# Optimization experiments

Hardware: AMD Instinct MI355X
Metric: run time of the kernel (lower is better)

The kernel has to match this reference:

```python
import jax, jax.numpy as jnp
import numpy as np


def setup_inputs() -> dict:
    key = jax.random.key(0)
    k1, k2, k3, k4, k5 = jax.random.split(key, 5)
    C, Cr = 512, 64  # in_channels, in_channels // 8
    B, W, H = 16, 64, 64
    x = jax.random.normal(k1, (B, C, W, H), dtype=jnp.float32)
    # 1x1 conv == pointwise linear over channels; store as [out, in]
    w1 = jax.random.normal(k2, (Cr, C), dtype=jnp.float32) * (1.0 / np.sqrt(C))
    b1 = jax.random.normal(k3, (Cr,), dtype=jnp.float32) * 0.01
    w2 = jax.random.normal(k4, (C, Cr), dtype=jnp.float32) * (1.0 / np.sqrt(Cr))
    b2 = jax.random.normal(k5, (C,), dtype=jnp.float32) * 0.01
    return {"x": x, "w1": w1, "b1": b1, "w2": w2, "b2": b2}


def reference(x, w1, b1, w2, b2):
    B, C, W, H = x.shape
    # conv1x1: channel reduction C -> C//8
    r = jnp.einsum('bchw,oc->bohw', x, w1) + b1[None, :, None, None]
    q = r.reshape(B, -1, W * H)                      # [B, C', N] query/key/value
    # channel-channel attention map [B, C', C'] (bmm(query, key^T))
    att = jnp.einsum('bcn,bdn->bcd', q, q)
    att = jax.nn.softmax(att, axis=-1)
    out = jnp.einsum('bcd,bdn->bcn', att, q)          # [B, C', N]
    out = out.reshape(B, -1, W, H)
    # conv_out: channel expansion C//8 -> C, plus residual
    out = jnp.einsum('bchw,oc->bohw', out, w2) + b2[None, :, None, None]
    return out + x
```

## Files before the change

kernel.cpp:

```cpp
#include <hip/hip_runtime.h>
#include <math.h>

#define NPIX 4096
#define CIN  512
#define CR   64
#define NB   16

typedef __bf16 bf16x8 __attribute__((ext_vector_type(8)));
typedef float  f32x4  __attribute__((ext_vector_type(4)));
typedef float  f32x16 __attribute__((ext_vector_type(16)));
typedef unsigned int uint;
typedef uint   uint4v __attribute__((ext_vector_type(4)));
typedef unsigned short ushort;

static const size_t Q_OFF   = 65536;
static const size_t QT_OFF  = Q_OFF  + (size_t)NB*CR*NPIX*2;
static const size_t ATT_OFF = QT_OFF + (size_t)NB*NPIX*CR*2;
static const size_t MB_OFF  = ATT_OFF + (size_t)NB*CR*CR*4;


static __device__ inline uint pk_bf16(float a, float b) {
    uint r;
    asm volatile("v_cvt_pk_bf16_f32 %0, %1, %2" : "=v"(r) : "v"(a), "v"(b));
    return r;
}

#define K1_LOAD(XV, WF, KS) do {                                             \
    int k0_ = (KS) * 32 + kg * 8;                                            \
    _Pragma("unroll")                                                        \
    for (int pf = 0; pf < 4; pf++) {                                         \
        const float* xp_ = xb + (size_t)k0_ * NPIX + pf * 16;                \
        _Pragma("unroll")                                                    \
        for (int j = 0; j < 8; j++) XV[pf][j] = xp_[(size_t)j * NPIX];       \
    }                                                                        \
    _Pragma("unroll")                                                        \
    for (int of = 0; of < 4; of++) {                                         \
        const float* wp_ = w1 + (size_t)(of * 16 + lo) * CIN + k0_;          \
        WF[of][0] = *(const f32x4*)wp_;                                      \
        WF[of][1] = *(const f32x4*)(wp_ + 4);                                \
    }                                                                        \
} while (0)

#define K1_COMPUTE(XV, WF) do {                                              \
    bf16x8 af_[4];                                                           \
    _Pragma("unroll")                                                        \
    for (int of = 0; of < 4; of++) {                                         \
        uint4v au_;                                                          \
        au_[0] = pk_bf16(WF[of][0][0], WF[of][0][1]);                        \
        au_[1] = pk_bf16(WF[of][0][2], WF[of][0][3]);                        \
        au_[2] = pk_bf16(WF[of][1][0], WF[of][1][1]);                        \
        au_[3] = pk_bf16(WF[of][1][2], WF[of][1][3]);                        \
        af_[of] = __builtin_bit_cast(bf16x8, au_);                           \
    }                                                                        \
    _Pragma("unroll")                                                        \
    for (int pf = 0; pf < 4; pf++) {                                         \
        uint4v bu_;                                                          \
        _Pragma("unroll")                                                    \
        for (int j = 0; j < 4; j++)                                          \
            bu_[j] = pk_bf16(XV[pf][2 * j], XV[pf][2 * j + 1]);              \
        bf16x8 bf_ = __builtin_bit_cast(bf16x8, bu_);                        \
        _Pragma("unroll")                                                    \
        for (int of = 0; of < 4; of++)                                       \
            acc[pf][of] = __builtin_amdgcn_mfma_f32_16x16x32_bf16(           \
                af_[of], bf_, acc[pf][of], 0, 0, 0);                         \
    }                                                                        \
} while (0)

__global__ __launch_bounds__(256) void k1_conv1(const float* __restrict__ x,
                                                const float* __restrict__ w1,
                                                const float* __restrict__ b1,
                                                ushort* __restrict__ q,
                                                uint2* __restrict__ qt4) {
    int b = blockIdx.y;
    int t = threadIdx.x;
    int wid = t >> 6, l = t & 63;
    int lo = l & 15, kg = l >> 4;
    int px0 = blockIdx.x * 256 + wid * 64;
    const float* xb = x + (size_t)b * CIN * NPIX + px0 + lo;

    f32x4 acc[4][4] = {};
    float xvA[4][8], xvB[4][8];
    f32x4 wfA[4][2], wfB[4][2];

    K1_LOAD(xvA, wfA, 0);
#pragma unroll
    for (int ks2 = 0; ks2 < 8; ks2++) {
        K1_LOAD(xvB, wfB, 2 * ks2 + 1);
        K1_COMPUTE(xvA, wfA);
        if (ks2 < 7) K1_LOAD(xvA, wfA, 2 * ks2 + 2);
        K1_COMPUTE(xvB, wfB);
    }

#pragma unroll
    for (int pf = 0; pf < 4; pf++) {
        int px = px0 + pf * 16 + lo;
        ushort* qb = q + (size_t)b * CR * NPIX + px;
        uint2* qt4b = qt4 + (((size_t)b * 256 + (px0 >> 4) + pf) * 4) * 64 + kg * 16 + lo;
#pragma unroll
        for (int of = 0; of < 4; of++) {
            int o = of * 16 + kg * 4;
            float v0 = acc[pf][of][0] + b1[o + 0];
            float v1 = acc[pf][of][1] + b1[o + 1];
            float v2 = acc[pf][of][2] + b1[o + 2];
            float v3 = acc[pf][of][3] + b1[o + 3];
            uint p0 = pk_bf16(v0, v1), p1 = pk_bf16(v2, v3);
            qb[(size_t)(o + 0) * NPIX] = (ushort)(p0 & 0xffff);
            qb[(size_t)(o + 1) * NPIX] = (ushort)(p0 >> 16);
            qb[(size_t)(o + 2) * NPIX] = (ushort)(p1 & 0xffff);
            qb[(size_t)(o + 3) * NPIX] = (ushort)(p1 >> 16);
            qt4b[of * 64] = make_uint2(p0, p1);
        }
    }
}

__global__ __launch_bounds__(1024) void k2_att(const ushort* __restrict__ q,
                                               float* __restrict__ att) {
    __shared__ float part[8][64][66];
    int b = blockIdx.x;
    int t = threadIdx.x;
    int w = t >> 6, l = t & 63;
    int lo = l & 15, kg = l >> 4;
    const ushort* qb = q + (size_t)b * CR * NPIX + w * 256;

    f32x4 acc[4][4] = {};
#pragma unroll 2
    for (int ks = 0; ks < 8; ks++) {
        bf16x8 fr[4];
#pragma unroll
        for (int cf = 0; cf < 4; cf++)
            fr[cf] = *(const bf16x8*)(qb + (size_t)(cf * 16 + lo) * NPIX + ks * 32 + kg * 8);
#pragma unroll
        for (int cf = 0; cf < 4; cf++)
#pragma unroll
            for (int df = 0; df < 4; df++)
                acc[cf][df] = __builtin_amdgcn_mfma_f32_16x16x32_bf16(fr[cf], fr[df], acc[cf][df], 0, 0, 0);
    }
    if (w < 8) {
#pragma unroll
        for (int cf = 0; cf < 4; cf++)
#pragma unroll
            for (int df = 0; df < 4; df++)
#pragma unroll
                for (int r = 0; r < 4; r++)
                    part[w][cf * 16 + kg * 4 + r][df * 16 + lo] = acc[cf][df][r];
    }
    __syncthreads();
    if (w >= 8) {
        int ws = w - 8;
#pragma unroll
        for (int cf = 0; cf < 4; cf++)
#pragma unroll
            for (int df = 0; df < 4; df++)
#pragma unroll
                for (int r = 0; r < 4; r++)
                    part[ws][cf * 16 + kg * 4 + r][df * 16 + lo] += acc[cf][df][r];
    }
    __syncthreads();

#pragma unroll
    for (int i = 0; i < 4; i++) {
        int c = w * 4 + i;
        float v = 0.f;
#pragma unroll
        for (int pw = 0; pw < 8; pw++) v += part[pw][c][l];
        float m = v;
#pragma unroll
        for (int s = 1; s < 64; s <<= 1) m = fmaxf(m, __shfl_xor(m, s, 64));
        float e = __expf(v - m);
        float ssum = e;
#pragma unroll
        for (int s = 1; s < 64; s <<= 1) ssum += __shfl_xor(ssum, s, 64);
        att[((size_t)b * CR + c) * CR + l] = e / ssum;
    }
}

__global__ __launch_bounds__(256) void k3_m(const float* __restrict__ w2,
                                            const float* __restrict__ att,
                                            ushort* __restrict__ mb) {
    int b = blockIdx.y;
    int c  = (blockIdx.x >> 2) * 256 + threadIdx.x;
    int dg = (blockIdx.x & 3) * 16;
    const float* ab  = att + (size_t)b * CR * CR + dg;
    const float* w2r = w2 + (size_t)c * CR;
    float acc[16];
#pragma unroll
    for (int j = 0; j < 16; j++) acc[j] = 0.f;
    for (int k = 0; k < CR; k++) {
        float wv = w2r[k];
#pragma unroll
        for (int j4 = 0; j4 < 4; j4++) {
            f32x4 av = *(const f32x4*)(ab + k * CR + j4 * 4);
#pragma unroll
            for (int u = 0; u < 4; u++)
                acc[j4 * 4 + u] = fmaf(wv, av[u], acc[j4 * 4 + u]);
        }
    }
    uint* mp = (uint*)(mb + ((size_t)b * CIN + c) * CR + dg);
#pragma unroll
    for (int i = 0; i < 8; i++)
        mp[i] = pk_bf16(acc[2 * i], acc[2 * i + 1]);
}

#define K4_LOAD(AF, XR, CC) do {                                             \
    int c0_ = (CC) * 32;                                                     \
    const ushort* mrow_ = mb + ((size_t)b * CIN + c0_ + l31) * CR;           \
    _Pragma("unroll")                                                        \
    for (int ks = 0; ks < 4; ks++)                                           \
        AF[ks] = *(const bf16x8*)(mrow_ + ks * 16 + lhi * 8);                \
    _Pragma("unroll")                                                        \
    for (int r = 0; r < 16; r++) {                                           \
        int rowD_ = (r & 3) + 8 * (r >> 2) + 4 * lhi;                        \
        XR[r] = x[((size_t)b * CIN + c0_ + rowD_) * NPIX + px];              \
    }                                                                        \
} while (0)

#define K4_STORE(AF, XR, CC) do {                                            \
    int c0_ = (CC) * 32;                                                     \
    f32x16 acc_ = {};                                                        \
    _Pragma("unroll")                                                        \
    for (int ks = 0; ks < 4; ks++)                                           \
        acc_ = __builtin_amdgcn_mfma_f32_32x32x16_bf16(AF[ks], bf[ks], acc_, 0, 0, 0); \
    _Pragma("unroll")                                                        \
    for (int r = 0; r < 16; r++) {                                           \
        int rowD_ = (r & 3) + 8 * (r >> 2) + 4 * lhi;                        \
        int c_ = c0_ + rowD_;                                                \
        size_t off_ = ((size_t)b * CIN + c_) * NPIX + px;                    \
        y[off_] = acc_[r] + b2[c_] + XR[r];                                  \
    }                                                                        \
} while (0)

__global__ __launch_bounds__(256) void k4_out(const uint2* __restrict__ qt4,
                                              const ushort* __restrict__ mb,
                                              const float* __restrict__ b2,
                                              const float* __restrict__ x,
                                              float* __restrict__ y) {
    int b = blockIdx.y;
    int t = threadIdx.x;
    int wid = t >> 6, l = t & 63;
    int l31 = l & 31, lhi = l >> 5;
    int pxblk = blockIdx.x * 128 + wid * 32;
    int px = pxblk + l31;
    const uint2* qt4b = qt4 + (size_t)b * 65536;
    int pxhi = (pxblk >> 4) + ((l >> 4) & 1);
    int pxlo = l & 15;
    int kg2 = lhi * 2;

    bf16x8 bf[4];
#pragma unroll
    for (int ks = 0; ks < 4; ks++) {
        const uint2* p_ = qt4b + (((size_t)pxhi * 4 + ks) * 4 + kg2) * 16 + pxlo;
        uint2 g0 = p_[0], g1 = p_[16];
        uint4v u; u[0] = g0.x; u[1] = g0.y; u[2] = g1.x; u[3] = g1.y;
        bf[ks] = __builtin_bit_cast(bf16x8, u);
    }

    bf16x8 afA[4], afB[4];
    float xrA[16], xrB[16];
    K4_LOAD(afA, xrA, 0);
#pragma unroll
    for (int i2 = 0; i2 < 8; i2++) {
        K4_LOAD(afB, xrB, 2 * i2 + 1);
        K4_STORE(afA, xrA, 2 * i2);
        if (i2 < 7) K4_LOAD(afA, xrA, 2 * i2 + 2);
        K4_STORE(afB, xrB, 2 * i2 + 1);
    }
}

extern "C" void kernel_launch(void* const* d_in, const int* in_sizes, int n_in,
                              void* d_out, int out_size, void* d_ws, size_t ws_size,
                              hipStream_t stream) {
    const float* x  = (const float*)d_in[0];
    const float* w1 = (const float*)d_in[1];
    const float* b1 = (const float*)d_in[2];
    const float* w2 = (const float*)d_in[3];
    const float* b2 = (const float*)d_in[4];
    float* y = (float*)d_out;
    char* ws = (char*)d_ws;

    ushort* q   = (ushort*)(ws + Q_OFF);
    uint2*  qt4 = (uint2*) (ws + QT_OFF);
    float*  att = (float*) (ws + ATT_OFF);
    ushort* mb  = (ushort*)(ws + MB_OFF);

    hipLaunchKernelGGL(k1_conv1, dim3(16, 16),  dim3(256),  0, stream, x, w1, b1, q, qt4);
    hipLaunchKernelGGL(k2_att,   dim3(16),      dim3(1024), 0, stream, q, att);
    hipLaunchKernelGGL(k3_m,     dim3(8, 16),   dim3(256),  0, stream, w2, att, mb);
    hipLaunchKernelGGL(k4_out,   dim3(32, 16),  dim3(256),  0, stream, qt4, mb, b2, x, y);
}
```

Measured before the change: 112.9 us.

## Split Gram-matrix kernel across row quarters to use more workgroups

The attention Gram kernel now launches 4x16 blocks of 512 threads instead of 16 blocks of 1024. Each block computes 16 rows of the 64x64 channel-attention matrix, and each wave reduces over a 512-pixel slice. This raises the number of active CUs from 16 to 64 and shrinks the shared-memory partials. The cost is that the full q tile is read four times per batch, and the two-phase accumulation across wave halves is dropped.

```diff
diff --git a/kernel.cpp b/kernel.cpp
--- a/kernel.cpp
+++ b/kernel.cpp
@@ -113,56 +113,41 @@
     }
 }
 
-__global__ __launch_bounds__(1024) void k2_att(const ushort* __restrict__ q,
-                                               float* __restrict__ att) {
-    __shared__ float part[8][64][66];
-    int b = blockIdx.x;
+__global__ __launch_bounds__(512) void k2_att(const ushort* __restrict__ q,
+                                              float* __restrict__ att) {
+    __shared__ float part[8][16][66];
+    int cq = blockIdx.x;
+    int b  = blockIdx.y;
     int t = threadIdx.x;
     int w = t >> 6, l = t & 63;
     int lo = l & 15, kg = l >> 4;
-    const ushort* qb = q + (size_t)b * CR * NPIX + w * 256;
-
-    f32x4 acc[4][4] = {};
-#pragma unroll 2
-    for (int ks = 0; ks < 8; ks++) {
+    const ushort* qb = q + (size_t)b * CR * NPIX + w * 512;
+
+    f32x4 acc[4] = {};
+    for (int ks = 0; ks < 16; ks++) {
+        int koff = ks * 32 + kg * 8;
+        bf16x8 fa = *(const bf16x8*)(qb + (size_t)(cq * 16 + lo) * NPIX + koff);
         bf16x8 fr[4];
 #pragma unroll
-        for (int cf = 0; cf < 4; cf++)
-            fr[cf] = *(const bf16x8*)(qb + (size_t)(cf * 16 + lo) * NPIX + ks * 32 + kg * 8);
-#pragma unroll
-        for (int cf = 0; cf < 4; cf++)
-#pragma unroll
-            for (int df = 0; df < 4; df++)
-                acc[cf][df] = __builtin_amdgcn_mfma_f32_16x16x32_bf16(fr[cf], fr[df], acc[cf][df], 0, 0, 0);
-    }
-    if (w < 8) {
-#pragma unroll
-        for (int cf = 0; cf < 4; cf++)
-#pragma unroll
-            for (int df = 0; df < 4; df++)
-#pragma unroll
-                for (int r = 0; r < 4; r++)
-                    part[w][cf * 16 + kg * 4 + r][df * 16 + lo] = acc[cf][df][r];
-    }
+        for (int df = 0; df < 4; df++)
+            fr[df] = *(const bf16x8*)(qb + (size_t)(df * 16 + lo) * NPIX + koff);
+#pragma unroll
+        for (int df = 0; df < 4; df++)
+            acc[df] = __builtin_amdgcn_mfma_f32_16x16x32_bf16(fa, fr[df], acc[df], 0, 0, 0);
+    }
+#pragma unroll
+    for (int df = 0; df < 4; df++)
+#pragma unroll
+        for (int r = 0; r < 4; r++)
+            part[w][kg * 4 + r][df * 16 + lo] = acc[df][r];
     __syncthreads();
-    if (w >= 8) {
-        int ws = w - 8;
-#pragma unroll
-        for (int cf = 0; cf < 4; cf++)
-#pragma unroll
-            for (int df = 0; df < 4; df++)
-#pragma unroll
-                for (int r = 0; r < 4; r++)
-                    part[ws][cf * 16 + kg * 4 + r][df * 16 + lo] += acc[cf][df][r];
-    }
-    __syncthreads();
-
-#pragma unroll
-    for (int i = 0; i < 4; i++) {
-        int c = w * 4 + i;
+
+#pragma unroll
+    for (int i = 0; i < 2; i++) {
+        int cl = w * 2 + i;
         float v = 0.f;
 #pragma unroll
-        for (int pw = 0; pw < 8; pw++) v += part[pw][c][l];
+        for (int pw = 0; pw < 8; pw++) v += part[pw][cl][l];
         float m = v;
 #pragma unroll
         for (int s = 1; s < 64; s <<= 1) m = fmaxf(m, __shfl_xor(m, s, 64));
@@ -170,7 +155,7 @@
         float ssum = e;
 #pragma unroll
         for (int s = 1; s < 64; s <<= 1) ssum += __shfl_xor(ssum, s, 64);
-        att[((size_t)b * CR + c) * CR + l] = e / ssum;
+        att[((size_t)b * CR + cq * 16 + cl) * CR + l] = e / ssum;
     }
 }
 
@@ -282,8 +267,8 @@
     float*  att = (float*) (ws + ATT_OFF);
     ushort* mb  = (ushort*)(ws + MB_OFF);
 
-    hipLaunchKernelGGL(k1_conv1, dim3(16, 16),  dim3(256),  0, stream, x, w1, b1, q, qt4);
-    hipLaunchKernelGGL(k2_att,   dim3(16),      dim3(1024), 0, stream, q, att);
-    hipLaunchKernelGGL(k3_m,     dim3(8, 16),   dim3(256),  0, stream, w2, att, mb);
-    hipLaunchKernelGGL(k4_out,   dim3(32, 16),  dim3(256),  0, stream, qt4, mb, b2, x, y);
-}
+    hipLaunchKernelGGL(k1_conv1, dim3(16, 16),  dim3(256), 0, stream, x, w1, b1, q, qt4);
+    hipLaunchKernelGGL(k2_att,   dim3(4, 16),   dim3(512), 0, stream, q, att);
+    hipLaunchKernelGGL(k3_m,     dim3(8, 16),   dim3(256), 0, stream, w2, att, mb);
+    hipLaunchKernelGGL(k4_out,   dim3(32, 16),  dim3(256), 0, stream, qt4, mb, b2, x, y);
+}
```

Measured after the change: 112.1 us. About the same (-0.7%).
